# Optimization experiments

Measured on AMD Instinct MI355X. Metric: run time of the kernel, lower is better.

## Reference

```python
import jax, jax.numpy as jnp
import numpy as np

D = 1024
W_SIZE = 512
K_ENGRAMS = 16
REPEAT = W_SIZE // K_ENGRAMS  # 32
LN_EPS = 1e-5


def setup_inputs() -> dict:
    key = jax.random.key(0)
    ks = jax.random.split(key, 6)
    B, NW = 4, 16
    engrams = jax.random.normal(ks[0], (B, NW, K_ENGRAMS, D), dtype=jnp.float32)
    pos_emb = 0.02 * jax.random.normal(ks[1], (1, 1, W_SIZE, D), dtype=jnp.float32)
    w1 = 0.02 * jax.random.normal(ks[2], (D, D), dtype=jnp.float32)
    b1 = jnp.zeros((D,), dtype=jnp.float32)
    w2 = 0.02 * jax.random.normal(ks[3], (D, D), dtype=jnp.float32)
    b2 = jnp.zeros((D,), dtype=jnp.float32)
    gamma = jnp.ones((D,), dtype=jnp.float32)
    beta = jnp.zeros((D,), dtype=jnp.float32)
    return {"engrams": engrams, "pos_emb": pos_emb, "w1": w1, "b1": b1,
            "w2": w2, "b2": b2, "gamma": gamma, "beta": beta}


def reference(engrams, pos_emb, w1, b1, w2, b2, gamma, beta):
    # (B, nw, K, d) -> (B, nw, W, d) via repeat_interleave along axis 2
    x = jnp.repeat(engrams, REPEAT, axis=2) + pos_emb
    # refine MLP: Linear -> GELU (exact) -> Linear, with residual
    h = jax.nn.gelu(jnp.einsum('bnwd,de->bnwe', x, w1.T) + b1, approximate=False)
    x = x + jnp.einsum('bnwd,de->bnwe', h, w2.T) + b2
    # LayerNorm over last dim
    mu = jnp.mean(x, axis=-1, keepdims=True)
    var = jnp.mean(jnp.square(x - mu), axis=-1, keepdims=True)
    return (x - mu) * jax.lax.rsqrt(var + LN_EPS) * gamma + beta
```

## Files before the change

kernel.cpp:

```cpp
#include <hip/hip_runtime.h>
#include <hip/hip_bf16.h>
#include <math.h>

#define D_DIM 1024
#define NROWS 32768
#define NE_ROWS 1024
#define A1_ROWS 1536

typedef __attribute__((ext_vector_type(8))) short bf16x8;
typedef __attribute__((ext_vector_type(4))) float f32x4;

static __device__ __forceinline__ ushort f2bf(float f) {
  union { float f; unsigned u; } un; un.f = f;
  unsigned u = un.u;
  unsigned r = u + 0x7fffu + ((u >> 16) & 1u);
  return (ushort)(r >> 16);
}

__global__ void cast_kernel(const float* __restrict__ src, ushort* __restrict__ dst, int n4) {
  int i = blockIdx.x * blockDim.x + threadIdx.x;
  if (i >= n4) return;
  float4 v = ((const float4*)src)[i];
  ushort4 o;
  o.x = f2bf(v.x); o.y = f2bf(v.y); o.z = f2bf(v.z); o.w = f2bf(v.w);
  ((ushort4*)dst)[i] = o;
}

__global__ __launch_bounds__(256) void gemm_bt(const ushort* __restrict__ A,
                                               const ushort* __restrict__ B,
                                               float* __restrict__ C,
                                               int M, int N, int K) {
  __shared__ ushort sA[128 * 64];
  __shared__ ushort sB[128 * 64];

  int nwg = gridDim.x;
  int bid = blockIdx.x;
  if ((nwg & 7) == 0) {
    int cpx = nwg >> 3;
    bid = (bid & 7) * cpx + (bid >> 3);
  }
  int ntn = N >> 7;
  int mt = bid / ntn, nt = bid % ntn;
  int brow = mt << 7, bcol = nt << 7;

  int tid = threadIdx.x;
  int wv = tid >> 6, lane = tid & 63;
  int wm = (wv >> 1) << 6, wn = (wv & 1) << 6;
  int lr = lane & 15, lk = lane >> 4;
  int srow = lane >> 3, scol = (lane & 7) << 3;

  f32x4 acc[4][4];
#pragma unroll
  for (int m = 0; m < 4; ++m)
#pragma unroll
    for (int n = 0; n < 4; ++n) acc[m][n] = (f32x4){0.f, 0.f, 0.f, 0.f};

  for (int k0 = 0; k0 < K; k0 += 64) {
    __syncthreads();
#pragma unroll
    for (int j = 0; j < 4; ++j) {
      int c = (wv << 2) + j;
      int row = (c << 3) + srow;
      const ushort* gA = A + (brow + row) * K + k0 + scol;
      const ushort* gB = B + (bcol + row) * K + k0 + scol;
      __builtin_amdgcn_global_load_lds(
          (const __attribute__((address_space(1))) unsigned int*)gA,
          (__attribute__((address_space(3))) unsigned int*)&sA[c << 9], 16, 0, 0);
      __builtin_amdgcn_global_load_lds(
          (const __attribute__((address_space(1))) unsigned int*)gB,
          (__attribute__((address_space(3))) unsigned int*)&sB[c << 9], 16, 0, 0);
    }
    __syncthreads();
#pragma unroll
    for (int kk = 0; kk < 2; ++kk) {
      bf16x8 af[4], bfr[4];
#pragma unroll
      for (int m = 0; m < 4; ++m)
        af[m] = *(const bf16x8*)&sA[(wm + (m << 4) + lr) * 64 + (kk << 5) + (lk << 3)];
#pragma unroll
      for (int n = 0; n < 4; ++n)
        bfr[n] = *(const bf16x8*)&sB[(wn + (n << 4) + lr) * 64 + (kk << 5) + (lk << 3)];
#pragma unroll
      for (int m = 0; m < 4; ++m)
#pragma unroll
        for (int n = 0; n < 4; ++n)
          acc[m][n] = __builtin_amdgcn_mfma_f32_16x16x32_bf16(af[m], bfr[n], acc[m][n], 0, 0, 0);
    }
  }

#pragma unroll
  for (int m = 0; m < 4; ++m)
#pragma unroll
    for (int n = 0; n < 4; ++n)
#pragma unroll
      for (int i = 0; i < 4; ++i) {
        int row = brow + wm + (m << 4) + (lk << 2) + i;
        int col = bcol + wn + (n << 4) + lr;
        C[(long)row * N + col] = acc[m][n][i];
      }
}

__global__ __launch_bounds__(256) void gelu_kernel(const float* __restrict__ xw1,
                                                   const float* __restrict__ b1,
                                                   ushort* __restrict__ h) {
  int r = blockIdx.x;
  int t = threadIdx.x;
  int bn = r >> 9;
  int w = r & 511;
  int er = bn * 16 + (w >> 5);
  float4 e = ((const float4*)(xw1 + er * D_DIM))[t];
  float4 p = ((const float4*)(xw1 + (NE_ROWS + w) * D_DIM))[t];
  float4 b = ((const float4*)b1)[t];
  float v[4] = {e.x + p.x + b.x, e.y + p.y + b.y, e.z + p.z + b.z, e.w + p.w + b.w};
  ushort4 o;
  float g0 = 0.5f * v[0] * (1.0f + erff(v[0] * 0.70710678118654752f));
  float g1 = 0.5f * v[1] * (1.0f + erff(v[1] * 0.70710678118654752f));
  float g2 = 0.5f * v[2] * (1.0f + erff(v[2] * 0.70710678118654752f));
  float g3 = 0.5f * v[3] * (1.0f + erff(v[3] * 0.70710678118654752f));
  o.x = f2bf(g0); o.y = f2bf(g1); o.z = f2bf(g2); o.w = f2bf(g3);
  ((ushort4*)(h + (long)r * D_DIM))[t] = o;
}

__global__ __launch_bounds__(256) void ln_kernel(const float* __restrict__ eng,
                                                 const float* __restrict__ pos,
                                                 const float* __restrict__ b2,
                                                 const float* __restrict__ gamma,
                                                 const float* __restrict__ beta,
                                                 float* __restrict__ out) {
  __shared__ float red[8];
  int r = blockIdx.x;
  int t = threadIdx.x;
  int bn = r >> 9, w = r & 511;
  int er = bn * 16 + (w >> 5);
  float4 xe = ((const float4*)(eng + er * D_DIM))[t];
  float4 xp = ((const float4*)(pos + w * D_DIM))[t];
  float4 y  = ((const float4*)(out + (long)r * D_DIM))[t];
  float4 bb = ((const float4*)b2)[t];
  float v0 = xe.x + xp.x + y.x + bb.x;
  float v1 = xe.y + xp.y + y.y + bb.y;
  float v2 = xe.z + xp.z + y.z + bb.z;
  float v3 = xe.w + xp.w + y.w + bb.w;
  float s  = v0 + v1 + v2 + v3;
  float sq = v0 * v0 + v1 * v1 + v2 * v2 + v3 * v3;
  int lane = t & 63, wv = t >> 6;
#pragma unroll
  for (int off = 32; off > 0; off >>= 1) {
    s  += __shfl_down(s, off);
    sq += __shfl_down(sq, off);
  }
  if (lane == 0) { red[wv] = s; red[4 + wv] = sq; }
  __syncthreads();
  float S  = red[0] + red[1] + red[2] + red[3];
  float SQ = red[4] + red[5] + red[6] + red[7];
  float mu = S * (1.0f / 1024.0f);
  float var = SQ * (1.0f / 1024.0f) - mu * mu;
  float rs = rsqrtf(var + 1e-5f);
  float4 g = ((const float4*)gamma)[t];
  float4 bt = ((const float4*)beta)[t];
  float4 o;
  o.x = (v0 - mu) * rs * g.x + bt.x;
  o.y = (v1 - mu) * rs * g.y + bt.y;
  o.z = (v2 - mu) * rs * g.z + bt.z;
  o.w = (v3 - mu) * rs * g.w + bt.w;
  ((float4*)(out + (long)r * D_DIM))[t] = o;
}

extern "C" void kernel_launch(void* const* d_in, const int* in_sizes, int n_in,
                              void* d_out, int out_size, void* d_ws, size_t ws_size,
                              hipStream_t stream) {
  const float* eng   = (const float*)d_in[0];
  const float* pos   = (const float*)d_in[1];
  const float* w1    = (const float*)d_in[2];
  const float* b1    = (const float*)d_in[3];
  const float* w2    = (const float*)d_in[4];
  const float* b2    = (const float*)d_in[5];
  const float* gamma = (const float*)d_in[6];
  const float* beta  = (const float*)d_in[7];
  float* out = (float*)d_out;

  char* ws = (char*)d_ws;
  ushort* w1b = (ushort*)(ws);
  ushort* w2b = (ushort*)(ws + (2u << 20));
  ushort* a1b = (ushort*)(ws + (4u << 20));
  float*  xw1 = (float*)(ws + (7u << 20));
  ushort* hb  = (ushort*)(ws + (13u << 20));

  cast_kernel<<<1024, 256, 0, stream>>>(w1, w1b, 1024 * 1024 / 4);
  cast_kernel<<<1024, 256, 0, stream>>>(w2, w2b, 1024 * 1024 / 4);
  cast_kernel<<<1024, 256, 0, stream>>>(eng, a1b, 1024 * 1024 / 4);
  cast_kernel<<<512, 256, 0, stream>>>(pos, a1b + 1024 * 1024, 512 * 1024 / 4);

  gemm_bt<<<(A1_ROWS / 128) * (D_DIM / 128), 256, 0, stream>>>(a1b, w1b, xw1,
                                                               A1_ROWS, D_DIM, D_DIM);

  gelu_kernel<<<NROWS, 256, 0, stream>>>(xw1, b1, hb);

  gemm_bt<<<(NROWS / 128) * (D_DIM / 128), 256, 0, stream>>>(hb, w2b, out,
                                                             NROWS, D_DIM, D_DIM);

  ln_kernel<<<NROWS, 256, 0, stream>>>(eng, pos, b2, gamma, beta, out);
}
```

Baseline: 211.0 us.

## Replace second GEMM with 256x256 tile, 4-stage pipelined LDS kernel

Adds a new GEMM kernel for the large second matmul that uses 256x256 tiles with 512 threads, a 4-deep multi-buffered async global-to-LDS prefetch tracked with vmcnt waits, XOR-swizzled LDS layout, and setprio around MFMA blocks. The aim is to hide global load latency behind MFMA work, cut LDS bank conflicts, and raise data reuse per tile compared with the 128x128 single-buffered kernel. It uses 128KB of LDS per block and more registers, which lowers occupancy, and the grid shrinks to 512 blocks.

```diff
diff --git a/kernel.cpp b/kernel.cpp
--- a/kernel.cpp
+++ b/kernel.cpp
@@ -98,6 +98,113 @@
         int col = bcol + wn + (n << 4) + lr;
         C[(long)row * N + col] = acc[m][n][i];
       }
+}
+
+__global__ __launch_bounds__(512, 2) void gemm_bt_256(const ushort* __restrict__ A,
+                                                      const ushort* __restrict__ B,
+                                                      float* __restrict__ C,
+                                                      int M, int N, int K) {
+  __shared__ ushort sA[4][8192];
+  __shared__ ushort sB[4][8192];
+
+  int nwg = gridDim.x;
+  int bid = blockIdx.x;
+  int cpx = nwg >> 3;
+  bid = (bid & 7) * cpx + (bid >> 3);
+  int ntn = N >> 8;
+  int mt = bid / ntn, nt = bid - mt * ntn;
+  long brow = (long)mt << 8;
+  int bcol = nt << 8;
+
+  int tid = threadIdx.x;
+  int wv = tid >> 6, lane = tid & 63;
+  int wr = wv >> 2, wc = wv & 3;
+  int wm = wr << 7, wn = wc << 6;
+  int lr = lane & 15, lk = lane >> 4;
+
+  int srow = tid >> 2;
+  int sslot = ((tid & 3) ^ (srow & 3)) << 3;
+  const ushort* aSrc = A + (brow + srow) * (long)K + sslot;
+  const ushort* bSrc = B + (long)(bcol + srow) * K + sslot;
+  int dBase = wv << 9;
+
+  int rdswz = (lk ^ (lr & 3)) << 3;
+  int aRead = (wm + lr) * 32 + rdswz;
+  int bRead = (wn + lr) * 32 + rdswz;
+
+  f32x4 acc[8][4];
+#pragma unroll
+  for (int m = 0; m < 8; ++m)
+#pragma unroll
+    for (int n = 0; n < 4; ++n) acc[m][n] = (f32x4){0.f, 0.f, 0.f, 0.f};
+
+  const int NT = K >> 5;
+
+#define STAGE(kt) do {                                                          \
+    int b_ = (kt) & 3; int k0_ = (kt) << 5;                                     \
+    _Pragma("unroll")                                                           \
+    for (int j = 0; j < 2; ++j) {                                               \
+      __builtin_amdgcn_global_load_lds(                                         \
+        (const __attribute__((address_space(1))) unsigned int*)(aSrc + k0_ + (long)(j << 7) * K), \
+        (__attribute__((address_space(3))) unsigned int*)&sA[b_][dBase + (j << 12)], 16, 0, 0);   \
+      __builtin_amdgcn_global_load_lds(                                         \
+        (const __attribute__((address_space(1))) unsigned int*)(bSrc + k0_ + (long)(j << 7) * K), \
+        (__attribute__((address_space(3))) unsigned int*)&sB[b_][dBase + (j << 12)], 16, 0, 0);   \
+    } } while (0)
+
+  STAGE(0); STAGE(1); STAGE(2);
+
+  for (int t = 0; t < NT; ++t) {
+    if (t + 3 < NT) {
+      STAGE(t + 3);
+      asm volatile("s_waitcnt vmcnt(12)" ::: "memory");
+    } else if (t == NT - 3) {
+      asm volatile("s_waitcnt vmcnt(8)" ::: "memory");
+    } else if (t == NT - 2) {
+      asm volatile("s_waitcnt vmcnt(4)" ::: "memory");
+    } else {
+      asm volatile("s_waitcnt vmcnt(0)" ::: "memory");
+    }
+    __builtin_amdgcn_s_barrier();
+
+    int b = t & 3;
+    const ushort* pA = &sA[b][aRead];
+    const ushort* pB = &sB[b][bRead];
+    bf16x8 bF[4], aF[4];
+#pragma unroll
+    for (int n = 0; n < 4; ++n) bF[n] = *(const bf16x8*)(pB + n * 512);
+#pragma unroll
+    for (int m = 0; m < 4; ++m) aF[m] = *(const bf16x8*)(pA + m * 512);
+    __builtin_amdgcn_s_setprio(1);
+#pragma unroll
+    for (int m = 0; m < 4; ++m)
+#pragma unroll
+      for (int n = 0; n < 4; ++n)
+        acc[m][n] = __builtin_amdgcn_mfma_f32_16x16x32_bf16(aF[m], bF[n], acc[m][n], 0, 0, 0);
+    __builtin_amdgcn_s_setprio(0);
+#pragma unroll
+    for (int m = 0; m < 4; ++m) aF[m] = *(const bf16x8*)(pA + (m + 4) * 512);
+    __builtin_amdgcn_s_setprio(1);
+#pragma unroll
+    for (int m = 0; m < 4; ++m)
+#pragma unroll
+      for (int n = 0; n < 4; ++n)
+        acc[m + 4][n] = __builtin_amdgcn_mfma_f32_16x16x32_bf16(aF[m], bF[n], acc[m + 4][n], 0, 0, 0);
+    __builtin_amdgcn_s_setprio(0);
+    __builtin_amdgcn_s_barrier();
+  }
+#undef STAGE
+
+#pragma unroll
+  for (int m = 0; m < 8; ++m)
+#pragma unroll
+    for (int n = 0; n < 4; ++n) {
+      long row = brow + wm + (m << 4) + (lk << 2);
+      int col = bcol + wn + (n << 4) + lr;
+      float* cp = C + row * N + col;
+#pragma unroll
+      for (int i = 0; i < 4; ++i) cp[(long)i * N] = acc[m][n][i];
+    }
 }
 
 __global__ __launch_bounds__(256) void gelu_kernel(const float* __restrict__ xw1,
@@ -195,8 +302,8 @@
 
   gelu_kernel<<<NROWS, 256, 0, stream>>>(xw1, b1, hb);
 
-  gemm_bt<<<(NROWS / 128) * (D_DIM / 128), 256, 0, stream>>>(hb, w2b, out,
-                                                             NROWS, D_DIM, D_DIM);
+  gemm_bt_256<<<(NROWS / 256) * (D_DIM / 256), 512, 0, stream>>>(hb, w2b, out,
+                                                                 NROWS, D_DIM, D_DIM);
 
   ln_kernel<<<NROWS, 256, 0, stream>>>(eng, pos, b2, gamma, beta, out);
 }
```

Result: faster. 201.4 us (-4.6%).

## Fuse GELU, second GEMM and LayerNorm into one full-row kernel

Applied to the files above, without the earlier changes.

Replaces the separate GELU, second GEMM and LayerNorm kernels with one kernel. Each block owns 64 full rows of 1024 columns, computes GELU on the fly into shared memory as the A operand, double-buffers W2 tiles, and does the residual add and LayerNorm in the epilogue. This removes the bf16 h intermediate and the fp32 output round trip. It also XOR-swizzles LDS layouts in the first GEMM to avoid bank conflicts. Costs are heavy register and LDS use (about 140KB LDS per block, 512 threads) and per-element GELU recomputed in the GEMM main loop.

```diff
diff --git a/kernel.cpp b/kernel.cpp
--- a/kernel.cpp
+++ b/kernel.cpp
@@ -6,6 +6,7 @@
 #define NROWS 32768
 #define NE_ROWS 1024
 #define A1_ROWS 1536
+#define NT 32
 
 typedef __attribute__((ext_vector_type(8))) short bf16x8;
 typedef __attribute__((ext_vector_type(4))) float f32x4;
@@ -15,6 +16,10 @@
   unsigned u = un.u;
   unsigned r = u + 0x7fffu + ((u >> 16) & 1u);
   return (ushort)(r >> 16);
+}
+
+static __device__ __forceinline__ float gelu_exact(float v) {
+  return 0.5f * v * (1.0f + erff(v * 0.70710678118654752f));
 }
 
 __global__ void cast_kernel(const float* __restrict__ src, ushort* __restrict__ dst, int n4) {
@@ -47,7 +52,8 @@
   int wv = tid >> 6, lane = tid & 63;
   int wm = (wv >> 1) << 6, wn = (wv & 1) << 6;
   int lr = lane & 15, lk = lane >> 4;
-  int srow = lane >> 3, scol = (lane & 7) << 3;
+  int srow = lane >> 3;
+  int scolsw = (((lane & 7) ^ ((lane >> 3) & 7)) << 3);
 
   f32x4 acc[4][4];
 #pragma unroll
@@ -61,8 +67,8 @@
     for (int j = 0; j < 4; ++j) {
       int c = (wv << 2) + j;
       int row = (c << 3) + srow;
-      const ushort* gA = A + (brow + row) * K + k0 + scol;
-      const ushort* gB = B + (bcol + row) * K + k0 + scol;
+      const ushort* gA = A + (brow + row) * K + k0 + scolsw;
+      const ushort* gB = B + (bcol + row) * K + k0 + scolsw;
       __builtin_amdgcn_global_load_lds(
           (const __attribute__((address_space(1))) unsigned int*)gA,
           (__attribute__((address_space(3))) unsigned int*)&sA[c << 9], 16, 0, 0);
@@ -73,13 +79,14 @@
     __syncthreads();
 #pragma unroll
     for (int kk = 0; kk < 2; ++kk) {
+      int rdoff = (((kk << 2) | lk) ^ (lr & 7)) << 3;
       bf16x8 af[4], bfr[4];
 #pragma unroll
       for (int m = 0; m < 4; ++m)
-        af[m] = *(const bf16x8*)&sA[(wm + (m << 4) + lr) * 64 + (kk << 5) + (lk << 3)];
+        af[m] = *(const bf16x8*)&sA[(wm + (m << 4) + lr) * 64 + rdoff];
 #pragma unroll
       for (int n = 0; n < 4; ++n)
-        bfr[n] = *(const bf16x8*)&sB[(wn + (n << 4) + lr) * 64 + (kk << 5) + (lk << 3)];
+        bfr[n] = *(const bf16x8*)&sB[(wn + (n << 4) + lr) * 64 + rdoff];
 #pragma unroll
       for (int m = 0; m < 4; ++m)
 #pragma unroll
@@ -100,69 +107,202 @@
       }
 }
 
-__global__ __launch_bounds__(256) void gelu_kernel(const float* __restrict__ xw1,
-                                                   const float* __restrict__ b1,
-                                                   ushort* __restrict__ h) {
-  int r = blockIdx.x;
-  int t = threadIdx.x;
-  int bn = r >> 9;
-  int w = r & 511;
-  int er = bn * 16 + (w >> 5);
-  float4 e = ((const float4*)(xw1 + er * D_DIM))[t];
-  float4 p = ((const float4*)(xw1 + (NE_ROWS + w) * D_DIM))[t];
-  float4 b = ((const float4*)b1)[t];
-  float v[4] = {e.x + p.x + b.x, e.y + p.y + b.y, e.z + p.z + b.z, e.w + p.w + b.w};
-  ushort4 o;
-  float g0 = 0.5f * v[0] * (1.0f + erff(v[0] * 0.70710678118654752f));
-  float g1 = 0.5f * v[1] * (1.0f + erff(v[1] * 0.70710678118654752f));
-  float g2 = 0.5f * v[2] * (1.0f + erff(v[2] * 0.70710678118654752f));
-  float g3 = 0.5f * v[3] * (1.0f + erff(v[3] * 0.70710678118654752f));
-  o.x = f2bf(g0); o.y = f2bf(g1); o.z = f2bf(g2); o.w = f2bf(g3);
-  ((ushort4*)(h + (long)r * D_DIM))[t] = o;
-}
-
-__global__ __launch_bounds__(256) void ln_kernel(const float* __restrict__ eng,
-                                                 const float* __restrict__ pos,
-                                                 const float* __restrict__ b2,
-                                                 const float* __restrict__ gamma,
-                                                 const float* __restrict__ beta,
-                                                 float* __restrict__ out) {
-  __shared__ float red[8];
-  int r = blockIdx.x;
-  int t = threadIdx.x;
-  int bn = r >> 9, w = r & 511;
-  int er = bn * 16 + (w >> 5);
-  float4 xe = ((const float4*)(eng + er * D_DIM))[t];
-  float4 xp = ((const float4*)(pos + w * D_DIM))[t];
-  float4 y  = ((const float4*)(out + (long)r * D_DIM))[t];
-  float4 bb = ((const float4*)b2)[t];
-  float v0 = xe.x + xp.x + y.x + bb.x;
-  float v1 = xe.y + xp.y + y.y + bb.y;
-  float v2 = xe.z + xp.z + y.z + bb.z;
-  float v3 = xe.w + xp.w + y.w + bb.w;
-  float s  = v0 + v1 + v2 + v3;
-  float sq = v0 * v0 + v1 * v1 + v2 * v2 + v3 * v3;
-  int lane = t & 63, wv = t >> 6;
-#pragma unroll
-  for (int off = 32; off > 0; off >>= 1) {
-    s  += __shfl_down(s, off);
-    sq += __shfl_down(sq, off);
-  }
-  if (lane == 0) { red[wv] = s; red[4 + wv] = sq; }
+__global__ __launch_bounds__(512, 2) void gemm2_ln(
+    const float* __restrict__ xw1,
+    const ushort* __restrict__ W2b,
+    const float* __restrict__ b1,
+    const float* __restrict__ eng, const float* __restrict__ pos,
+    const float* __restrict__ b2, const float* __restrict__ gamma_,
+    const float* __restrict__ beta_, float* __restrict__ out) {
+  __shared__ ushort sB0[2][16384];
+  __shared__ ushort sB1[2][16384];
+  __shared__ ushort sAs[2][2048];
+  __shared__ float red[64][8][2];
+  __shared__ float musd[64][2];
+
+  int bid = blockIdx.x;
+  bid = (bid & 7) * 64 + (bid >> 3);
+  long brow = (long)bid << 6;
+  int w0 = (int)(brow & 511);
+  int bn = (int)(brow >> 9);
+  int er0 = bn * 16 + (w0 >> 5);
+
+  int tid = threadIdx.x;
+  int wv = tid >> 6, lane = tid & 63;
+  int lr = lane & 15, lk = lane >> 4;
+
+  int bRow = tid >> 2;
+  int bSlot = (((tid & 3) ^ ((tid >> 3) & 3)) << 3);
+  int dOff = wv << 9;
+
+  int aRow = tid >> 3, aQ = tid & 7;
+  const float* aEP = xw1 + ((size_t)(er0 + (aRow >> 5)) << 10) + (aQ << 2);
+  const float* aPP = xw1 + ((size_t)(NE_ROWS + w0 + aRow) << 10) + (aQ << 2);
+  const float* b1P = b1 + (aQ << 2);
+  int aWr = aRow * 32 + ((((aQ >> 1) ^ ((aRow >> 1) & 3)) << 3)) + ((aQ & 1) << 2);
+
+  int rdswz = (lk ^ ((lr >> 1) & 3)) << 3;
+  int aRd = lr * 32 + rdswz;
+  int bRd = (wv << 11) + lr * 32 + rdswz;
+
+  f32x4 acc[4][2][4];
+#pragma unroll
+  for (int m = 0; m < 4; ++m)
+#pragma unroll
+    for (int h = 0; h < 2; ++h)
+#pragma unroll
+      for (int f = 0; f < 4; ++f) acc[m][h][f] = (f32x4){0.f, 0.f, 0.f, 0.f};
+
+#define STAGE_B(arr, hofs, buf_, k0_) do {                                        \
+    _Pragma("unroll")                                                             \
+    for (int j = 0; j < 4; ++j) {                                                 \
+      __builtin_amdgcn_global_load_lds(                                           \
+        (const __attribute__((address_space(1))) unsigned int*)                   \
+          (W2b + ((size_t)((hofs) + j * 128 + bRow) << 10) + (k0_) + bSlot),      \
+        (__attribute__((address_space(3))) unsigned int*)&arr[buf_][(j << 12) + dOff], \
+        16, 0, 0);                                                                \
+    } } while (0)
+
+  {
+    float4 ae = *(const float4*)aEP;
+    float4 ap = *(const float4*)aPP;
+    float4 ab = *(const float4*)b1P;
+    STAGE_B(sB0, 0, 0, 0);
+    STAGE_B(sB1, 512, 0, 0);
+    asm volatile("s_waitcnt vmcnt(0)" ::: "memory");
+    ushort4 o;
+    o.x = f2bf(gelu_exact(ae.x + ap.x + ab.x));
+    o.y = f2bf(gelu_exact(ae.y + ap.y + ab.y));
+    o.z = f2bf(gelu_exact(ae.z + ap.z + ab.z));
+    o.w = f2bf(gelu_exact(ae.w + ap.w + ab.w));
+    *(ushort4*)&sAs[0][aWr] = o;
+    asm volatile("s_waitcnt lgkmcnt(0)" ::: "memory");
+    __builtin_amdgcn_s_barrier();
+  }
+
+  for (int t = 0; t < NT - 1; ++t) {
+    const int cur = t & 1, nxt = cur ^ 1;
+    const int k1 = (t + 1) << 5;
+    float4 ae = *(const float4*)(aEP + k1);
+    float4 ap = *(const float4*)(aPP + k1);
+    float4 ab = *(const float4*)(b1P + k1);
+    STAGE_B(sB0, 0, nxt, k1);
+    bf16x8 aF[4], bF[4];
+#pragma unroll
+    for (int m = 0; m < 4; ++m) aF[m] = *(const bf16x8*)&sAs[cur][aRd + m * 512];
+#pragma unroll
+    for (int f = 0; f < 4; ++f) bF[f] = *(const bf16x8*)&sB0[cur][bRd + f * 512];
+    __builtin_amdgcn_s_setprio(1);
+#pragma unroll
+    for (int m = 0; m < 4; ++m)
+#pragma unroll
+      for (int f = 0; f < 4; ++f)
+        acc[m][0][f] = __builtin_amdgcn_mfma_f32_16x16x32_bf16(aF[m], bF[f], acc[m][0][f], 0, 0, 0);
+    __builtin_amdgcn_s_setprio(0);
+    asm volatile("s_waitcnt vmcnt(0)" ::: "memory");
+    ushort4 o;
+    o.x = f2bf(gelu_exact(ae.x + ap.x + ab.x));
+    o.y = f2bf(gelu_exact(ae.y + ap.y + ab.y));
+    o.z = f2bf(gelu_exact(ae.z + ap.z + ab.z));
+    o.w = f2bf(gelu_exact(ae.w + ap.w + ab.w));
+    *(ushort4*)&sAs[nxt][aWr] = o;
+    asm volatile("s_waitcnt lgkmcnt(0)" ::: "memory");
+    __builtin_amdgcn_s_barrier();
+    STAGE_B(sB1, 512, nxt, k1);
+#pragma unroll
+    for (int f = 0; f < 4; ++f) bF[f] = *(const bf16x8*)&sB1[cur][bRd + f * 512];
+    __builtin_amdgcn_s_setprio(1);
+#pragma unroll
+    for (int m = 0; m < 4; ++m)
+#pragma unroll
+      for (int f = 0; f < 4; ++f)
+        acc[m][1][f] = __builtin_amdgcn_mfma_f32_16x16x32_bf16(aF[m], bF[f], acc[m][1][f], 0, 0, 0);
+    __builtin_amdgcn_s_setprio(0);
+  }
+  {
+    const int cur = (NT - 1) & 1;
+    bf16x8 aF[4], bF[4];
+#pragma unroll
+    for (int m = 0; m < 4; ++m) aF[m] = *(const bf16x8*)&sAs[cur][aRd + m * 512];
+#pragma unroll
+    for (int f = 0; f < 4; ++f) bF[f] = *(const bf16x8*)&sB0[cur][bRd + f * 512];
+#pragma unroll
+    for (int m = 0; m < 4; ++m)
+#pragma unroll
+      for (int f = 0; f < 4; ++f)
+        acc[m][0][f] = __builtin_amdgcn_mfma_f32_16x16x32_bf16(aF[m], bF[f], acc[m][0][f], 0, 0, 0);
+    asm volatile("s_waitcnt vmcnt(0)" ::: "memory");
+    __builtin_amdgcn_s_barrier();
+#pragma unroll
+    for (int f = 0; f < 4; ++f) bF[f] = *(const bf16x8*)&sB1[cur][bRd + f * 512];
+#pragma unroll
+    for (int m = 0; m < 4; ++m)
+#pragma unroll
+      for (int f = 0; f < 4; ++f)
+        acc[m][1][f] = __builtin_amdgcn_mfma_f32_16x16x32_bf16(aF[m], bF[f], acc[m][1][f], 0, 0, 0);
+  }
+#undef STAGE_B
+
+  float cb2[8], cg[8], cbt[8];
+#pragma unroll
+  for (int h = 0; h < 2; ++h)
+#pragma unroll
+    for (int f = 0; f < 4; ++f) {
+      int col = h * 512 + (wv << 6) + (f << 4) + lr;
+      cb2[h * 4 + f] = b2[col];
+      cg[h * 4 + f] = gamma_[col];
+      cbt[h * 4 + f] = beta_[col];
+    }
+#pragma unroll
+  for (int m = 0; m < 4; ++m) {
+    const float* eRow = eng + ((size_t)(er0 + (m >> 1)) << 10);
+#pragma unroll
+    for (int i = 0; i < 4; ++i) {
+      int rl = (m << 4) + (lk << 2) + i;
+      const float* pRow = pos + ((size_t)(w0 + rl) << 10);
+      float s = 0.f, q = 0.f;
+#pragma unroll
+      for (int h = 0; h < 2; ++h)
+#pragma unroll
+        for (int f = 0; f < 4; ++f) {
+          int col = h * 512 + (wv << 6) + (f << 4) + lr;
+          float v = acc[m][h][f][i] + eRow[col] + pRow[col] + cb2[h * 4 + f];
+          acc[m][h][f][i] = v;
+          s += v; q += v * v;
+        }
+      s += __shfl_xor(s, 1); q += __shfl_xor(q, 1);
+      s += __shfl_xor(s, 2); q += __shfl_xor(q, 2);
+      s += __shfl_xor(s, 4); q += __shfl_xor(q, 4);
+      s += __shfl_xor(s, 8); q += __shfl_xor(q, 8);
+      if (lr == 0) { red[rl][wv][0] = s; red[rl][wv][1] = q; }
+    }
+  }
   __syncthreads();
-  float S  = red[0] + red[1] + red[2] + red[3];
-  float SQ = red[4] + red[5] + red[6] + red[7];
-  float mu = S * (1.0f / 1024.0f);
-  float var = SQ * (1.0f / 1024.0f) - mu * mu;
-  float rs = rsqrtf(var + 1e-5f);
-  float4 g = ((const float4*)gamma)[t];
-  float4 bt = ((const float4*)beta)[t];
-  float4 o;
-  o.x = (v0 - mu) * rs * g.x + bt.x;
-  o.y = (v1 - mu) * rs * g.y + bt.y;
-  o.z = (v2 - mu) * rs * g.z + bt.z;
-  o.w = (v3 - mu) * rs * g.w + bt.w;
-  ((float4*)(out + (long)r * D_DIM))[t] = o;
+  if (wv == 0) {
+    float S = 0.f, Q = 0.f;
+#pragma unroll
+    for (int j = 0; j < 8; ++j) { S += red[lane][j][0]; Q += red[lane][j][1]; }
+    float mu = S * (1.0f / 1024.0f);
+    float var = Q * (1.0f / 1024.0f) - mu * mu;
+    musd[lane][0] = mu;
+    musd[lane][1] = rsqrtf(var + 1e-5f);
+  }
+  __syncthreads();
+#pragma unroll
+  for (int m = 0; m < 4; ++m)
+#pragma unroll
+    for (int i = 0; i < 4; ++i) {
+      int rl = (m << 4) + (lk << 2) + i;
+      float mu = musd[rl][0], rs = musd[rl][1];
+      float* orow = out + ((brow + rl) << 10);
+#pragma unroll
+      for (int h = 0; h < 2; ++h)
+#pragma unroll
+        for (int f = 0; f < 4; ++f) {
+          int col = h * 512 + (wv << 6) + (f << 4) + lr;
+          orow[col] = (acc[m][h][f][i] - mu) * rs * cg[h * 4 + f] + cbt[h * 4 + f];
+        }
+    }
 }
 
 extern "C" void kernel_launch(void* const* d_in, const int* in_sizes, int n_in,
@@ -183,7 +323,6 @@
   ushort* w2b = (ushort*)(ws + (2u << 20));
   ushort* a1b = (ushort*)(ws + (4u << 20));
   float*  xw1 = (float*)(ws + (7u << 20));
-  ushort* hb  = (ushort*)(ws + (13u << 20));
 
   cast_kernel<<<1024, 256, 0, stream>>>(w1, w1b, 1024 * 1024 / 4);
   cast_kernel<<<1024, 256, 0, stream>>>(w2, w2b, 1024 * 1024 / 4);
@@ -193,10 +332,5 @@
   gemm_bt<<<(A1_ROWS / 128) * (D_DIM / 128), 256, 0, stream>>>(a1b, w1b, xw1,
                                                                A1_ROWS, D_DIM, D_DIM);
 
-  gelu_kernel<<<NROWS, 256, 0, stream>>>(xw1, b1, hb);
-
-  gemm_bt<<<(NROWS / 128) * (D_DIM / 128), 256, 0, stream>>>(hb, w2b, out,
-                                                             NROWS, D_DIM, D_DIM);
-
-  ln_kernel<<<NROWS, 256, 0, stream>>>(eng, pos, b2, gamma, beta, out);
-}
+  gemm2_ln<<<NROWS / 64, 512, 0, stream>>>(xw1, w2b, b1, eng, pos, b2, gamma, beta, out);
+}
```

New measurement: 205.8 us. 2.5% less time.
